# Kernel optimization log

Measured on AMD Instinct MI355X. Metric: run time of the kernel, lower is better.

Reference implementation:

```python
import jax, jax.numpy as jnp
import numpy as np

D = 128          # embed_d
T = 10           # MAX_NEIGHBORS
L = 2            # n_layers
B = 4096
ND, FD = 20000, 2048
NG, FG = 20000, 1024
NC, FC = 10000, 512


def setup_inputs() -> dict:
    key = jax.random.key(0)
    ks = jax.random.split(key, 18)
    inp = {
        'drug_feats': jax.random.normal(ks[0], (ND, FD), jnp.float32),
        'gene_feats': jax.random.normal(ks[1], (NG, FG), jnp.float32),
        'cell_feats': jax.random.normal(ks[2], (NC, FC), jnp.float32),
        'Wd': jax.random.normal(ks[3], (FD, D), jnp.float32) / np.sqrt(FD),
        'bd': jnp.zeros((D,), jnp.float32),
        'Wg': jax.random.normal(ks[4], (FG, D), jnp.float32) / np.sqrt(FG),
        'bg': jnp.zeros((D,), jnp.float32),
        'Wc': jax.random.normal(ks[5], (FC, D), jnp.float32) / np.sqrt(FC),
        'bc': jnp.zeros((D,), jnp.float32),
        'gru_W': jax.random.normal(ks[6], (L, 3, D, 3 * D), jnp.float32) / np.sqrt(D),
        'gru_U': jax.random.normal(ks[7], (L, 3, D, 3 * D), jnp.float32) / np.sqrt(D),
        'gru_b': jnp.zeros((L, 3, 3 * D), jnp.float32),
        'att': jax.random.normal(ks[8], (L, 2 * D), jnp.float32) / np.sqrt(2 * D),
        'ids': jax.random.randint(ks[9], (B,), 0, ND, jnp.int32),
        # neighbor ids in [-1, N-1]; -1 == PAD_VALUE
        'neigh_drug': jax.random.randint(ks[10], (B, T), 0, ND + 1, jnp.int32) - 1,
        'neigh_gene': jax.random.randint(ks[11], (B, T), 0, NG + 1, jnp.int32) - 1,
        'neigh_cell': jax.random.randint(ks[12], (B, T), 0, NC + 1, jnp.int32) - 1,
    }
    return inp


def _proj_gather(table, W, b, idx):
    # gather raw features by id (PAD -> zeros) then project, matching
    # conteng_agg + masked scatter in node_het_agg.
    mask = (idx >= 0)                              # [B, T]
    safe = jnp.clip(idx, 0, None)
    f = table[safe] @ W + b                        # [B, T, D]
    return f * mask[..., None].astype(f.dtype), mask


def _gru_seq(x, W, U, b):
    # x: [B, T, D]; torch-style GRU, returns all hidden states [B, T, D]
    xw = jnp.einsum('btd,de->bte', x, W) + b       # [B, T, 3D]
    h0 = jnp.zeros((x.shape[0], U.shape[0]), x.dtype)

    def step(h, xt):
        hu = h @ U
        xz, xr, xn = jnp.split(xt, 3, axis=-1)
        hz, hr, hn = jnp.split(hu, 3, axis=-1)
        z = jax.nn.sigmoid(xz + hz)
        r = jax.nn.sigmoid(xr + hr)
        n = jnp.tanh(xn + r * hn)
        h = (1.0 - z) * n + z * h
        return h, h

    _, hs = jax.lax.scan(step, h0, jnp.swapaxes(xw, 0, 1))
    return jnp.swapaxes(hs, 0, 1)


def reference(drug_feats, gene_feats, cell_feats, Wd, bd, Wg, bg, Wc, bc,
              gru_W, gru_U, gru_b, att, ids, neigh_drug, neigh_gene, neigh_cell):
    # self embeddings: conteng_agg(batch_ids, drug_type)
    h = drug_feats[ids] @ Wd + bd                  # [B, D]

    # neighbor content features are the layer-0 projections every layer
    # (the torch code recomputes conteng_agg per layer; result is identical)
    neigh = [
        _proj_gather(drug_feats, Wd, bd, neigh_drug),
        _proj_gather(gene_feats, Wg, bg, neigh_gene),
        _proj_gather(cell_feats, Wc, bc, neigh_cell),
    ]

    for l in range(L):
        cands = [h]
        for t, (nf, mask) in enumerate(neigh):
            out = _gru_seq(nf, gru_W[l, t], gru_U[l, t], gru_b[l, t])  # [B,T,D]
            m = mask.astype(out.dtype)
            cnt = jnp.maximum(m.sum(-1, keepdims=True), 1.0)
            cands.append((out * m[..., None]).sum(1) / cnt)            # [B,D]
        C = jnp.stack(cands, axis=1)                                   # [B,4,D]
        cat = jnp.concatenate(
            [jnp.broadcast_to(h[:, None, :], C.shape), C], axis=-1)    # [B,4,2D]
        w = jax.nn.softmax(jax.nn.leaky_relu(cat @ att[l]), axis=-1)   # [B,4]
        h = jnp.einsum('bk,bkd->bd', w, C)
    return h
```

## Files before the change

kernel.cpp:

```cpp
#include <hip/hip_runtime.h>
#include <stdint.h>


typedef short bf16x8 __attribute__((ext_vector_type(8)));
typedef float f32x4  __attribute__((ext_vector_type(4)));

__device__ __forceinline__ short f2bf(float f) {
  union { float f; unsigned u; } v; v.f = f;
  unsigned r = (v.u + 0x7fffu + ((v.u >> 16) & 1u)) >> 16;
  return (short)r;
}
__device__ __forceinline__ float b2f(short s) {
  union { float f; unsigned u; } v; v.u = ((unsigned)(unsigned short)s) << 16;
  return v.f;
}
__device__ __forceinline__ f32x4 mfma_bf16(bf16x8 a, bf16x8 b, f32x4 c) {
  return __builtin_amdgcn_mfma_f32_16x16x32_bf16(a, b, c, 0, 0, 0);
}

struct PrepW { const float* src[3]; short* dst[3]; int K[3]; };

__global__ __launch_bounds__(256) void prep_w(PrepW a) {
  const int y = blockIdx.y;
  const int K = a.K[y];
  int i = blockIdx.x * 256 + threadIdx.x;
  if (i < K * 128) {
    int k = i >> 7, n = i & 127;
    a.dst[y][(size_t)n * K + k] = f2bf(a.src[y][i]);
  }
}

__global__ __launch_bounds__(256) void prep_gru(const float* __restrict__ W,
                                                const float* __restrict__ U,
                                                short* __restrict__ dW,
                                                short* __restrict__ dU) {
  const int y = blockIdx.y;
  const float* s = (y < 6) ? W + (size_t)y * 49152 : U + (size_t)(y - 6) * 49152;
  short* d       = (y < 6) ? dW + (size_t)y * 49152 : dU + (size_t)(y - 6) * 49152;
  int i = blockIdx.x * 256 + threadIdx.x;
  if (i < 49152) {
    int k = i / 384, n = i - k * 384;
    d[(size_t)n * 128 + k] = f2bf(s[i]);
  }
}

struct ProjA {
  const float* A[3]; const short* Wt[3]; const float* bias[3];
  short* Pb[3]; float* Pf[3]; int M[3]; int K[3];
};

__global__ __launch_bounds__(256, 5) void proj_all(ProjA p) {
  const int y = blockIdx.y;
  const int M = p.M[y];
  const int m0 = blockIdx.x * 32;
  if (m0 >= M) return;
  const int K = p.K[y];
  const float* A    = p.A[y];
  const short* Wt   = p.Wt[y];
  const float* bias = p.bias[y];
  short* Pb         = p.Pb[y];
  float* Pf         = p.Pf[y];

  __shared__ alignas(16) short As[2][32][136];
  const int tid  = threadIdx.x;
  const int lane = tid & 63;
  const int w    = tid >> 6;
  const int wc   = w * 32;
  const int quad = lane >> 4;
  const int ln   = lane & 15;
  const int kq   = quad * 8;

  const int arow = tid >> 3;
  const int akc  = (tid & 7) * 16;

  const int kIters = K >> 7;
  const int krot   = blockIdx.x % kIters;
  const int gr     = m0 + arow;
  const bool aok   = gr < M;
  const float* arp = A + (size_t)gr * K + akc;
  const short* brp0 = Wt + (size_t)(wc + ln) * K + kq;
  const short* brp1 = Wt + (size_t)(wc + 16 + ln) * K + kq;

  float4 areg[4];
  auto loadA = [&](int k0) {
    if (aok) {
      const float4* ptr = (const float4*)(arp + k0);
      areg[0] = ptr[0]; areg[1] = ptr[1]; areg[2] = ptr[2]; areg[3] = ptr[3];
    } else {
      float4 z = {0.f, 0.f, 0.f, 0.f};
      areg[0] = z; areg[1] = z; areg[2] = z; areg[3] = z;
    }
  };
  auto cvtStore = [&](int buf) {
    bf16x8 v0, v1;
    v0[0]=f2bf(areg[0].x); v0[1]=f2bf(areg[0].y); v0[2]=f2bf(areg[0].z); v0[3]=f2bf(areg[0].w);
    v0[4]=f2bf(areg[1].x); v0[5]=f2bf(areg[1].y); v0[6]=f2bf(areg[1].z); v0[7]=f2bf(areg[1].w);
    v1[0]=f2bf(areg[2].x); v1[1]=f2bf(areg[2].y); v1[2]=f2bf(areg[2].z); v1[3]=f2bf(areg[2].w);
    v1[4]=f2bf(areg[3].x); v1[5]=f2bf(areg[3].y); v1[6]=f2bf(areg[3].z); v1[7]=f2bf(areg[3].w);
    *(bf16x8*)&As[buf][arow][akc]     = v0;
    *(bf16x8*)&As[buf][arow][akc + 8] = v1;
  };

  f32x4 acc[2][2];
#pragma unroll
  for (int i = 0; i < 2; i++)
#pragma unroll
    for (int j = 0; j < 2; j++) acc[i][j] = (f32x4){0.f, 0.f, 0.f, 0.f};

  loadA(krot << 7);
  cvtStore(0);
  __syncthreads();

  for (int it = 0; it < kIters; it++) {
    int ks = krot + it; if (ks >= kIters) ks -= kIters;
    const int k0 = ks << 7;
    if (it + 1 < kIters) {
      int kn = ks + 1; if (kn >= kIters) kn -= kIters;
      loadA(kn << 7);
    }
    bf16x8 bfr[2][4];
#pragma unroll
    for (int kt = 0; kt < 4; kt++) {
      bfr[0][kt] = *(const bf16x8*)(brp0 + k0 + kt * 32);
      bfr[1][kt] = *(const bf16x8*)(brp1 + k0 + kt * 32);
    }
    const int buf = it & 1;
#pragma unroll
    for (int kt = 0; kt < 4; kt++) {
      bf16x8 af0 = *(const bf16x8*)&As[buf][ln][kt * 32 + kq];
      bf16x8 af1 = *(const bf16x8*)&As[buf][16 + ln][kt * 32 + kq];
      acc[0][0] = mfma_bf16(af0, bfr[0][kt], acc[0][0]);
      acc[0][1] = mfma_bf16(af0, bfr[1][kt], acc[0][1]);
      acc[1][0] = mfma_bf16(af1, bfr[0][kt], acc[1][0]);
      acc[1][1] = mfma_bf16(af1, bfr[1][kt], acc[1][1]);
    }
    if (it + 1 < kIters) cvtStore(buf ^ 1);
    __syncthreads();
  }

#pragma unroll
  for (int mi = 0; mi < 2; mi++)
#pragma unroll
    for (int nj = 0; nj < 2; nj++) {
      const int col = wc + nj * 16 + ln;
      const float bv = bias[col];
#pragma unroll
      for (int r = 0; r < 4; r++) {
        const int row = m0 + mi * 16 + quad * 4 + r;
        if (row < M) {
          const float v = acc[mi][nj][r] + bv;
          if (Pb) Pb[(size_t)row * 128 + col] = f2bf(v);
          if (Pf) Pf[(size_t)row * 128 + col] = v;
        }
      }
    }
}

__global__ __launch_bounds__(256) void gather_h0(const float* __restrict__ Pd,
                                                 const int* __restrict__ ids,
                                                 float* __restrict__ h) {
  int i = blockIdx.x * 256 + threadIdx.x;
  int b = i >> 7, d = i & 127;
  h[i] = Pd[(size_t)ids[b] * 128 + d];
}

__global__ __launch_bounds__(256) void xw_all(
    const short* __restrict__ P0, const short* __restrict__ P1,
    const short* __restrict__ P2, const int* __restrict__ n0,
    const int* __restrict__ n1, const int* __restrict__ n2,
    const short* __restrict__ gWt_all, const float* __restrict__ grub_all,
    short* __restrict__ xwT_base, int s_base) {
  const int s  = s_base + blockIdx.z;
  const int ty = s - (s / 3) * 3;
  const short* Pb  = (ty == 0) ? P0 : (ty == 1) ? P1 : P2;
  const int*   nbr = (ty == 0) ? n0 : (ty == 1) ? n1 : n2;
  const short* Wts = gWt_all + (size_t)s * 49152;
  const float* gbs = grub_all + (size_t)s * 384;
  short* xwT = xwT_base + (size_t)blockIdx.z * 40960 * 384;

  __shared__ alignas(16) short As[64][136];
  __shared__ alignas(16) short Bs[128][136];
  const int tid  = threadIdx.x;
  const int lane = tid & 63;
  const int w    = tid >> 6;
  const int wr   = (w >> 1) * 32;
  const int wc   = (w & 1) * 64;
  const int quad = lane >> 4;
  const int ln   = lane & 15;
  const int m0    = blockIdx.x * 64;
  const int nbase = blockIdx.y * 128;

  {
    const int row = tid >> 2;
    const int kc  = (tid & 3) * 32;
    const int idx = nbr[m0 + row];
    if (idx >= 0) {
      const short* p = Pb + (size_t)idx * 128 + kc;
#pragma unroll
      for (int i = 0; i < 4; i++)
        *(bf16x8*)&As[row][kc + i * 8] = *(const bf16x8*)(p + i * 8);
    } else {
      bf16x8 zv;
#pragma unroll
      for (int i = 0; i < 8; i++) zv[i] = 0;
#pragma unroll
      for (int i = 0; i < 4; i++) *(bf16x8*)&As[row][kc + i * 8] = zv;
    }
  }
  {
    const int n  = tid >> 1;
    const int kc = (tid & 1) * 64;
    const short* p = Wts + (size_t)(nbase + n) * 128 + kc;
#pragma unroll
    for (int i = 0; i < 8; i++)
      *(bf16x8*)&Bs[n][kc + i * 8] = *(const bf16x8*)(p + i * 8);
  }
  __syncthreads();

  f32x4 acc[2][4];
#pragma unroll
  for (int i = 0; i < 2; i++)
#pragma unroll
    for (int j = 0; j < 4; j++) acc[i][j] = (f32x4){0.f, 0.f, 0.f, 0.f};

#pragma unroll
  for (int kt = 0; kt < 4; kt++) {
    bf16x8 af[2], bfr[4];
#pragma unroll
    for (int mi = 0; mi < 2; mi++)
      af[mi] = *(const bf16x8*)&As[wr + mi * 16 + ln][kt * 32 + quad * 8];
#pragma unroll
    for (int nj = 0; nj < 4; nj++)
      bfr[nj] = *(const bf16x8*)&Bs[wc + nj * 16 + ln][kt * 32 + quad * 8];
#pragma unroll
    for (int mi = 0; mi < 2; mi++)
#pragma unroll
      for (int nj = 0; nj < 4; nj++)
        acc[mi][nj] = mfma_bf16(af[mi], bfr[nj], acc[mi][nj]);
  }

#pragma unroll
  for (int mi = 0; mi < 2; mi++)
#pragma unroll
    for (int nj = 0; nj < 4; nj++) {
      const int col = wc + nj * 16 + ln;
      const float bv = gbs[nbase + col];
#pragma unroll
      for (int r = 0; r < 4; r++) {
        const int rt   = m0 + wr + mi * 16 + quad * 4 + r;
        const int grow = rt / 10;
        const int st   = rt - grow * 10;
        xwT[((size_t)st * 4096 + grow) * 384 + nbase + col] =
            f2bf(acc[mi][nj][r] + bv);
      }
    }
}

__global__ __launch_bounds__(256) void scan_all(
    const short* __restrict__ xwT_base, const short* __restrict__ Ut_base,
    const int* __restrict__ n0, const int* __restrict__ n1,
    const int* __restrict__ n2, float* __restrict__ out_base, int s_base) {
  const int sz = blockIdx.y;
  const int s  = s_base + sz;
  const int ty = s - (s / 3) * 3;
  const short* xwT = xwT_base + (size_t)sz * 40960 * 384;
  const short* Utz = Ut_base + (size_t)s * 49152;
  const int*   nbr = (ty == 0) ? n0 : (ty == 1) ? n1 : n2;
  float* outp = out_base + (size_t)sz * 4096 * 128;

  __shared__ alignas(16) short hs[16][128];
  __shared__ alignas(16) short xls[16][392];
  __shared__ float mask_s[16][10];
  __shared__ float cinv[16];

  const int tid  = threadIdx.x;
  const int lane = tid & 63;
  const int w    = tid >> 6;
  const int nb   = w * 32;
  const int quad = lane >> 4;
  const int ln   = lane & 15;
  const int r0   = blockIdx.x * 16;

  if (tid < 160) {
    int i = tid / 10, tt = tid % 10;
    mask_s[i][tt] = (nbr[(r0 + i) * 10 + tt] >= 0) ? 1.f : 0.f;
  }
  {
    short* hf = &hs[0][0];
    for (int i = tid; i < 16 * 128; i += 256) hf[i] = 0;
  }
  __syncthreads();
  if (tid < 16) {
    float sm = 0.f;
    for (int tt = 0; tt < 10; tt++) sm += mask_s[tid][tt];
    cinv[tid] = 1.f / fmaxf(sm, 1.f);
  }

  bf16x8 u[3][2][4];
#pragma unroll
  for (int g = 0; g < 3; g++)
#pragma unroll
    for (int jj = 0; jj < 2; jj++)
#pragma unroll
      for (int kt = 0; kt < 4; kt++)
        u[g][jj][kt] = *(const bf16x8*)(Utz +
            (size_t)(g * 128 + nb + jj * 16 + ln) * 128 + kt * 32 + quad * 8);

  int srow[3], scol[3];
#pragma unroll
  for (int j = 0; j < 3; j++) {
    const int o = tid * 24 + j * 8;
    srow[j] = o / 384;
    scol[j] = o - srow[j] * 384;
  }

  float hreg[2][4], oacc[2][4];
#pragma unroll
  for (int jj = 0; jj < 2; jj++)
#pragma unroll
    for (int r = 0; r < 4; r++) { hreg[jj][r] = 0.f; oacc[jj][r] = 0.f; }

  __syncthreads();

  for (int st = 0; st < 10; st++) {
    bf16x8 a[4];
#pragma unroll
    for (int kt = 0; kt < 4; kt++)
      a[kt] = *(const bf16x8*)&hs[ln][kt * 32 + quad * 8];

    const short* src = xwT + ((size_t)st * 4096 + r0) * 384;
    bf16x8 xrg[3];
#pragma unroll
    for (int j = 0; j < 3; j++)
      xrg[j] = *(const bf16x8*)(src + tid * 24 + j * 8);

    f32x4 hu[3][2];
#pragma unroll
    for (int g = 0; g < 3; g++)
#pragma unroll
      for (int jj = 0; jj < 2; jj++) hu[g][jj] = (f32x4){0.f, 0.f, 0.f, 0.f};
#pragma unroll
    for (int kt = 0; kt < 4; kt++)
#pragma unroll
      for (int g = 0; g < 3; g++)
#pragma unroll
        for (int jj = 0; jj < 2; jj++)
          hu[g][jj] = mfma_bf16(a[kt], u[g][jj][kt], hu[g][jj]);

#pragma unroll
    for (int j = 0; j < 3; j++)
      *(bf16x8*)&xls[srow[j]][scol[j]] = xrg[j];
    __syncthreads();

#pragma unroll
    for (int jj = 0; jj < 2; jj++) {
      const int col = nb + jj * 16 + ln;
#pragma unroll
      for (int r = 0; r < 4; r++) {
        const int row = quad * 4 + r;
        const float xz = b2f(xls[row][col]);
        const float xr = b2f(xls[row][col + 128]);
        const float xn = b2f(xls[row][col + 256]);
        const float zg = 1.f / (1.f + __expf(-(xz + hu[0][jj][r])));
        const float rg = 1.f / (1.f + __expf(-(xr + hu[1][jj][r])));
        const float pn = xn + rg * hu[2][jj][r];
        const float e2 = __expf(2.f * pn);
        const float n  = (e2 - 1.f) / (e2 + 1.f);
        const float hn = (1.f - zg) * n + zg * hreg[jj][r];
        hreg[jj][r] = hn;
        oacc[jj][r] += hn * mask_s[row][st];
        hs[row][col] = f2bf(hn);
      }
    }
    __syncthreads();
  }

#pragma unroll
  for (int jj = 0; jj < 2; jj++)
#pragma unroll
    for (int r = 0; r < 4; r++) {
      const int row = quad * 4 + r;
      outp[(size_t)(r0 + row) * 128 + nb + jj * 16 + ln] =
          oacc[jj][r] * cinv[row];
    }
}

__global__ __launch_bounds__(256) void attn_kernel(
    const float* __restrict__ hin, const float* __restrict__ cand,
    const float* __restrict__ att, float* __restrict__ hout) {
  const int tid  = threadIdx.x;
  const int lane = tid & 63;
  const int w    = tid >> 6;
  const int gb   = blockIdx.x * 4 + w;

  const float ah0 = att[lane],       ah1 = att[lane + 64];
  const float ac0 = att[128 + lane], ac1 = att[192 + lane];

  float c0[4], c1[4];
  c0[0] = hin[(size_t)gb * 128 + lane];
  c1[0] = hin[(size_t)gb * 128 + 64 + lane];
#pragma unroll
  for (int k = 1; k < 4; k++) {
    const float* p = cand + (size_t)(k - 1) * 4096 * 128 + (size_t)gb * 128;
    c0[k] = p[lane]; c1[k] = p[64 + lane];
  }

  float sh = ah0 * c0[0] + ah1 * c1[0];
#pragma unroll
  for (int m = 1; m < 64; m <<= 1) sh += __shfl_xor(sh, m);

  float e[4];
#pragma unroll
  for (int k = 0; k < 4; k++) {
    float sv = ac0 * c0[k] + ac1 * c1[k];
#pragma unroll
    for (int m = 1; m < 64; m <<= 1) sv += __shfl_xor(sv, m);
    sv += sh;
    e[k] = (sv > 0.f) ? sv : 0.01f * sv;
  }
  const float mx = fmaxf(fmaxf(e[0], e[1]), fmaxf(e[2], e[3]));
  float wk[4], wsum = 0.f;
#pragma unroll
  for (int k = 0; k < 4; k++) { wk[k] = __expf(e[k] - mx); wsum += wk[k]; }
  const float inv = 1.f / wsum;
  float o0 = 0.f, o1 = 0.f;
#pragma unroll
  for (int k = 0; k < 4; k++) { o0 += wk[k] * c0[k]; o1 += wk[k] * c1[k]; }
  hout[(size_t)gb * 128 + lane]      = o0 * inv;
  hout[(size_t)gb * 128 + 64 + lane] = o1 * inv;
}

extern "C" void kernel_launch(void* const* d_in, const int* in_sizes, int n_in,
                              void* d_out, int out_size, void* d_ws, size_t ws_size,
                              hipStream_t stream) {
  const float* drug = (const float*)d_in[0];
  const float* gene = (const float*)d_in[1];
  const float* cell = (const float*)d_in[2];
  const float* Wd   = (const float*)d_in[3];
  const float* bd   = (const float*)d_in[4];
  const float* Wg   = (const float*)d_in[5];
  const float* bg   = (const float*)d_in[6];
  const float* Wc   = (const float*)d_in[7];
  const float* bc   = (const float*)d_in[8];
  const float* gruW = (const float*)d_in[9];
  const float* gruU = (const float*)d_in[10];
  const float* grub = (const float*)d_in[11];
  const float* att  = (const float*)d_in[12];
  const int* ids    = (const int*)d_in[13];
  const int* nbr[3] = {(const int*)d_in[14], (const int*)d_in[15],
                       (const int*)d_in[16]};

  const size_t XW_SLOT   = (size_t)40960 * 384;
  const size_t CAND_SLOT = (size_t)4096 * 128;

  const size_t need_big =
      (size_t)20000 * 128 * 4 + (size_t)20000 * 128 * 2 +
      (size_t)20000 * 128 * 2 + (size_t)10000 * 128 * 2 +
      (size_t)4096 * 128 * 4 + 6 * CAND_SLOT * 4 + 6 * XW_SLOT * 2 +
      (size_t)2048 * 128 * 2 + (size_t)1024 * 128 * 2 + (size_t)512 * 128 * 2 +
      2 * (size_t)6 * 384 * 128 * 2 + 16384 ;
  const bool big = ws_size >= need_big;

  char* ws = (char*)d_ws;
  auto alloc = [&](size_t bytes) {
    void* p = ws; ws += (bytes + 255) & ~(size_t)255; return p;
  };
  float* Pdf  = (float*)alloc((size_t)20000 * 128 * 4);
  short* Pdb  = (short*)alloc((size_t)20000 * 128 * 2);
  short* Pgb  = (short*)alloc((size_t)20000 * 128 * 2);
  short* Pcb  = (short*)alloc((size_t)10000 * 128 * 2);
  float* h    = (float*)alloc((size_t)4096 * 128 * 4);
  float* cand = (float*)alloc((big ? 6 : 3) * CAND_SLOT * 4);
  short* xwb  = (short*)alloc((big ? 6 : 1) * XW_SLOT * 2);
  short* Wdt  = (short*)alloc((size_t)2048 * 128 * 2);
  short* Wgt  = (short*)alloc((size_t)1024 * 128 * 2);
  short* Wct  = (short*)alloc((size_t)512 * 128 * 2);
  short* gWt  = (short*)alloc((size_t)6 * 384 * 128 * 2);
  short* Ut   = (short*)alloc((size_t)6 * 384 * 128 * 2);

  {
    PrepW pw;
    pw.src[0] = Wd;  pw.dst[0] = Wdt; pw.K[0] = 2048;
    pw.src[1] = Wg;  pw.dst[1] = Wgt; pw.K[1] = 1024;
    pw.src[2] = Wc;  pw.dst[2] = Wct; pw.K[2] = 512;
    prep_w<<<dim3(1024, 3), 256, 0, stream>>>(pw);
  }
  prep_gru<<<dim3(192, 12), 256, 0, stream>>>(gruW, gruU, gWt, Ut);

  {
    ProjA pa;
    pa.A[0] = drug; pa.Wt[0] = Wdt; pa.bias[0] = bd;
    pa.Pb[0] = Pdb; pa.Pf[0] = Pdf; pa.M[0] = 20000; pa.K[0] = 2048;
    pa.A[1] = gene; pa.Wt[1] = Wgt; pa.bias[1] = bg;
    pa.Pb[1] = Pgb; pa.Pf[1] = nullptr; pa.M[1] = 20000; pa.K[1] = 1024;
    pa.A[2] = cell; pa.Wt[2] = Wct; pa.bias[2] = bc;
    pa.Pb[2] = Pcb; pa.Pf[2] = nullptr; pa.M[2] = 10000; pa.K[2] = 512;
    proj_all<<<dim3(625, 3), 256, 0, stream>>>(pa);
  }
  gather_h0<<<2048, 256, 0, stream>>>(Pdf, ids, h);

  if (big) {
    xw_all<<<dim3(640, 3, 6), 256, 0, stream>>>(
        Pdb, Pgb, Pcb, nbr[0], nbr[1], nbr[2], gWt, grub, xwb, 0);
    scan_all<<<dim3(256, 6), 256, 0, stream>>>(
        xwb, Ut, nbr[0], nbr[1], nbr[2], cand, 0);
    attn_kernel<<<1024, 256, 0, stream>>>(h, cand, att, h);
    attn_kernel<<<1024, 256, 0, stream>>>(
        h, cand + 3 * CAND_SLOT, att + 256, (float*)d_out);
  } else {
    for (int l = 0; l < 2; l++) {
      for (int t = 0; t < 3; t++) {
        const int s = l * 3 + t;
        xw_all<<<dim3(640, 3, 1), 256, 0, stream>>>(
            Pdb, Pgb, Pcb, nbr[0], nbr[1], nbr[2], gWt, grub, xwb, s);
        scan_all<<<dim3(256, 1), 256, 0, stream>>>(
            xwb, Ut, nbr[0], nbr[1], nbr[2], cand + (size_t)t * CAND_SLOT, s);
      }
      attn_kernel<<<1024, 256, 0, stream>>>(
          h, cand, att + l * 256, (l == 1) ? (float*)d_out : h);
    }
  }
}
```

Before: 549.7 us.

## Restructure projection GEMM: 16-row tiles, templated K, deeper prefetch, packed bf16 convert

The projection kernel now uses 16-row tiles with twice as many blocks and is templated on the K-iteration count, so each table gets a fully unrolled loop. A-tiles are prefetched two steps ahead and B fragments one step ahead in register banks, and fp32-to-bf16 conversion uses the packed v_cvt_pk_bf16_f32 instruction. The aim is to hide global-load latency and raise parallelism on the memory-bound feature projection. In exchange, each block reuses its B fragments across fewer rows, register pressure rises, and the row-bounds checks are dropped, which relies on M being a multiple of 16.

```diff
diff --git a/kernel.cpp b/kernel.cpp
--- a/kernel.cpp
+++ b/kernel.cpp
@@ -13,6 +13,11 @@
 __device__ __forceinline__ float b2f(short s) {
   union { float f; unsigned u; } v; v.u = ((unsigned)(unsigned short)s) << 16;
   return v.f;
+}
+__device__ __forceinline__ unsigned cvt_pk_bf16(float lo, float hi) {
+  unsigned r;
+  asm("v_cvt_pk_bf16_f32 %0, %1, %2" : "=v"(r) : "v"(lo), "v"(hi));
+  return r;
 }
 __device__ __forceinline__ f32x4 mfma_bf16(bf16x8 a, bf16x8 b, f32x4 c) {
   return __builtin_amdgcn_mfma_f32_16x16x32_bf16(a, b, c, 0, 0, 0);
@@ -46,22 +51,17 @@
 
 struct ProjA {
   const float* A[3]; const short* Wt[3]; const float* bias[3];
-  short* Pb[3]; float* Pf[3]; int M[3]; int K[3];
+  short* Pb[3]; float* Pf[3]; int M[3];
 };
 
-__global__ __launch_bounds__(256, 5) void proj_all(ProjA p) {
-  const int y = blockIdx.y;
-  const int M = p.M[y];
-  const int m0 = blockIdx.x * 32;
+template<int KI>
+__device__ __forceinline__ void proj_body(
+    const float* __restrict__ A, const short* __restrict__ Wt,
+    const float* __restrict__ bias, short* __restrict__ Pb,
+    float* __restrict__ Pf, int M, short (*As)[16][136]) {
+  const int K  = KI << 7;
+  const int m0 = blockIdx.x * 16;
   if (m0 >= M) return;
-  const int K = p.K[y];
-  const float* A    = p.A[y];
-  const short* Wt   = p.Wt[y];
-  const float* bias = p.bias[y];
-  short* Pb         = p.Pb[y];
-  float* Pf         = p.Pf[y];
-
-  __shared__ alignas(16) short As[2][32][136];
   const int tid  = threadIdx.x;
   const int lane = tid & 63;
   const int w    = tid >> 6;
@@ -70,90 +70,85 @@
   const int ln   = lane & 15;
   const int kq   = quad * 8;
 
-  const int arow = tid >> 3;
-  const int akc  = (tid & 7) * 16;
-
-  const int kIters = K >> 7;
-  const int krot   = blockIdx.x % kIters;
-  const int gr     = m0 + arow;
-  const bool aok   = gr < M;
-  const float* arp = A + (size_t)gr * K + akc;
+  const int arow = tid >> 4;
+  const int akc  = (tid & 15) * 8;
+  const int krot = blockIdx.x % KI;
+
+  const float* arp  = A + (size_t)(m0 + arow) * K + akc;
   const short* brp0 = Wt + (size_t)(wc + ln) * K + kq;
   const short* brp1 = Wt + (size_t)(wc + 16 + ln) * K + kq;
 
-  float4 areg[4];
-  auto loadA = [&](int k0) {
-    if (aok) {
-      const float4* ptr = (const float4*)(arp + k0);
-      areg[0] = ptr[0]; areg[1] = ptr[1]; areg[2] = ptr[2]; areg[3] = ptr[3];
-    } else {
-      float4 z = {0.f, 0.f, 0.f, 0.f};
-      areg[0] = z; areg[1] = z; areg[2] = z; areg[3] = z;
-    }
+  float4 ar[2][2];
+  bf16x8 b0[2][4], b1[2][4];
+  f32x4 acc0 = (f32x4){0.f, 0.f, 0.f, 0.f};
+  f32x4 acc1 = (f32x4){0.f, 0.f, 0.f, 0.f};
+
+  auto kof = [&](int i) {
+    int ks = krot + i; if (ks >= KI) ks -= KI; return ks << 7;
   };
-  auto cvtStore = [&](int buf) {
-    bf16x8 v0, v1;
-    v0[0]=f2bf(areg[0].x); v0[1]=f2bf(areg[0].y); v0[2]=f2bf(areg[0].z); v0[3]=f2bf(areg[0].w);
-    v0[4]=f2bf(areg[1].x); v0[5]=f2bf(areg[1].y); v0[6]=f2bf(areg[1].z); v0[7]=f2bf(areg[1].w);
-    v1[0]=f2bf(areg[2].x); v1[1]=f2bf(areg[2].y); v1[2]=f2bf(areg[2].z); v1[3]=f2bf(areg[2].w);
-    v1[4]=f2bf(areg[3].x); v1[5]=f2bf(areg[3].y); v1[6]=f2bf(areg[3].z); v1[7]=f2bf(areg[3].w);
-    *(bf16x8*)&As[buf][arow][akc]     = v0;
-    *(bf16x8*)&As[buf][arow][akc + 8] = v1;
+  auto loadA = [&](int bank, int k0) {
+    const float4* p = (const float4*)(arp + k0);
+    ar[bank][0] = p[0]; ar[bank][1] = p[1];
   };
-
-  f32x4 acc[2][2];
-#pragma unroll
-  for (int i = 0; i < 2; i++)
-#pragma unroll
-    for (int j = 0; j < 2; j++) acc[i][j] = (f32x4){0.f, 0.f, 0.f, 0.f};
-
-  loadA(krot << 7);
-  cvtStore(0);
+  auto loadB = [&](int bank, int k0) {
+#pragma unroll
+    for (int kt = 0; kt < 4; kt++) {
+      b0[bank][kt] = *(const bf16x8*)(brp0 + k0 + kt * 32);
+      b1[bank][kt] = *(const bf16x8*)(brp1 + k0 + kt * 32);
+    }
+  };
+  auto cvtStore = [&](int buf, int bank) {
+    union { unsigned u[4]; bf16x8 v; } pk;
+    pk.u[0] = cvt_pk_bf16(ar[bank][0].x, ar[bank][0].y);
+    pk.u[1] = cvt_pk_bf16(ar[bank][0].z, ar[bank][0].w);
+    pk.u[2] = cvt_pk_bf16(ar[bank][1].x, ar[bank][1].y);
+    pk.u[3] = cvt_pk_bf16(ar[bank][1].z, ar[bank][1].w);
+    *(bf16x8*)&As[buf][arow][akc] = pk.v;
+  };
+
+  loadA(0, kof(0));
+  loadA(1, kof(1));
+  loadB(0, kof(0));
+  cvtStore(0, 0);
   __syncthreads();
 
-  for (int it = 0; it < kIters; it++) {
-    int ks = krot + it; if (ks >= kIters) ks -= kIters;
-    const int k0 = ks << 7;
-    if (it + 1 < kIters) {
-      int kn = ks + 1; if (kn >= kIters) kn -= kIters;
-      loadA(kn << 7);
-    }
-    bf16x8 bfr[2][4];
+#pragma unroll
+  for (int i = 0; i < KI; i++) {
+    if (i + 1 < KI) loadB((i + 1) & 1, kof(i + 1));
+    if (i + 2 < KI) loadA(i & 1, kof(i + 2));
 #pragma unroll
     for (int kt = 0; kt < 4; kt++) {
-      bfr[0][kt] = *(const bf16x8*)(brp0 + k0 + kt * 32);
-      bfr[1][kt] = *(const bf16x8*)(brp1 + k0 + kt * 32);
-    }
-    const int buf = it & 1;
-#pragma unroll
-    for (int kt = 0; kt < 4; kt++) {
-      bf16x8 af0 = *(const bf16x8*)&As[buf][ln][kt * 32 + kq];
-      bf16x8 af1 = *(const bf16x8*)&As[buf][16 + ln][kt * 32 + kq];
-      acc[0][0] = mfma_bf16(af0, bfr[0][kt], acc[0][0]);
-      acc[0][1] = mfma_bf16(af0, bfr[1][kt], acc[0][1]);
-      acc[1][0] = mfma_bf16(af1, bfr[0][kt], acc[1][0]);
-      acc[1][1] = mfma_bf16(af1, bfr[1][kt], acc[1][1]);
-    }
-    if (it + 1 < kIters) cvtStore(buf ^ 1);
+      bf16x8 af = *(const bf16x8*)&As[i & 1][ln][kt * 32 + kq];
+      acc0 = mfma_bf16(af, b0[i & 1][kt], acc0);
+      acc1 = mfma_bf16(af, b1[i & 1][kt], acc1);
+    }
+    if (i + 1 < KI) cvtStore((i + 1) & 1, (i + 1) & 1);
     __syncthreads();
   }
 
 #pragma unroll
-  for (int mi = 0; mi < 2; mi++)
-#pragma unroll
-    for (int nj = 0; nj < 2; nj++) {
-      const int col = wc + nj * 16 + ln;
-      const float bv = bias[col];
-#pragma unroll
-      for (int r = 0; r < 4; r++) {
-        const int row = m0 + mi * 16 + quad * 4 + r;
-        if (row < M) {
-          const float v = acc[mi][nj][r] + bv;
-          if (Pb) Pb[(size_t)row * 128 + col] = f2bf(v);
-          if (Pf) Pf[(size_t)row * 128 + col] = v;
-        }
-      }
-    }
+  for (int nj = 0; nj < 2; nj++) {
+    const int col = wc + nj * 16 + ln;
+    const float bv = bias[col];
+#pragma unroll
+    for (int r = 0; r < 4; r++) {
+      const int row = m0 + quad * 4 + r;
+      const float v = (nj ? acc1[r] : acc0[r]) + bv;
+      if (Pb) Pb[(size_t)row * 128 + col] = f2bf(v);
+      if (Pf) Pf[(size_t)row * 128 + col] = v;
+    }
+  }
+}
+
+__global__ __launch_bounds__(256, 4) void proj_all(ProjA p) {
+  __shared__ alignas(16) short As[2][16][136];
+  const int y = blockIdx.y;
+  if (y == 0)
+    proj_body<16>(p.A[0], p.Wt[0], p.bias[0], p.Pb[0], p.Pf[0], p.M[0], As);
+  else if (y == 1)
+    proj_body<8>(p.A[1], p.Wt[1], p.bias[1], p.Pb[1], p.Pf[1], p.M[1], As);
+  else
+    proj_body<4>(p.A[2], p.Wt[2], p.bias[2], p.Pb[2], p.Pf[2], p.M[2], As);
 }
 
 __global__ __launch_bounds__(256) void gather_h0(const float* __restrict__ Pd,
@@ -490,12 +485,12 @@
   {
     ProjA pa;
     pa.A[0] = drug; pa.Wt[0] = Wdt; pa.bias[0] = bd;
-    pa.Pb[0] = Pdb; pa.Pf[0] = Pdf; pa.M[0] = 20000; pa.K[0] = 2048;
+    pa.Pb[0] = Pdb; pa.Pf[0] = Pdf; pa.M[0] = 20000;
     pa.A[1] = gene; pa.Wt[1] = Wgt; pa.bias[1] = bg;
-    pa.Pb[1] = Pgb; pa.Pf[1] = nullptr; pa.M[1] = 20000; pa.K[1] = 1024;
+    pa.Pb[1] = Pgb; pa.Pf[1] = nullptr; pa.M[1] = 20000;
     pa.A[2] = cell; pa.Wt[2] = Wct; pa.bias[2] = bc;
-    pa.Pb[2] = Pcb; pa.Pf[2] = nullptr; pa.M[2] = 10000; pa.K[2] = 512;
-    proj_all<<<dim3(625, 3), 256, 0, stream>>>(pa);
+    pa.Pb[2] = Pcb; pa.Pf[2] = nullptr; pa.M[2] = 10000;
+    proj_all<<<dim3(1250, 3), 256, 0, stream>>>(pa);
   }
   gather_h0<<<2048, 256, 0, stream>>>(Pdf, ids, h);
 
```

Measured after the change: 602.5 us. +9.6%, slower.
